# Optimization experiments

Measured on AMD Instinct MI355X. Metric: run time of the kernel, lower is better.

The kernel has to match this reference:

```python
import jax, jax.numpy as jnp
import numpy as np

N, K, S, E = 8192, 15, 128, 24
H, A, HID, DEPTH, MIX = 8, 32, 512, 3, 10
RBF_MAX, RBF_K = 20.0, 16


def _norm(v):
    return v / (jnp.linalg.norm(v, axis=-1, keepdims=True) + 1e-8)


def orientation_frames(pos):
    # pos: [N,3] CA coords -> per-residue local rotation frames [N,3,3]
    u = _norm(pos[1:] - pos[:-1])
    b = _norm(u[:-1] - u[1:])
    n = _norm(jnp.cross(u[:-1], u[1:]))
    o = jnp.cross(b, n)
    R = jnp.stack([b, n, o], axis=-1)              # [N-2,3,3]
    return jnp.concatenate([R[:1], R, R[-1:]], 0)  # edge-pad to [N,3,3]


def rot_to_quat(R):
    m00, m11, m22 = R[..., 0, 0], R[..., 1, 1], R[..., 2, 2]
    def comp(t, a, b):
        return 0.5 * jnp.sqrt(jnp.maximum(1e-8, t)) * jnp.sign(a - b)
    qw = 0.5 * jnp.sqrt(jnp.maximum(1e-8, 1. + m00 + m11 + m22))
    qx = comp(1. + m00 - m11 - m22, R[..., 2, 1], R[..., 1, 2])
    qy = comp(1. - m00 + m11 - m22, R[..., 0, 2], R[..., 2, 0])
    qz = comp(1. - m00 - m11 + m22, R[..., 1, 0], R[..., 0, 1])
    return jnp.stack([qw, qx, qy, qz], axis=-1)


def rbf_expand(d):
    mu = jnp.linspace(0., RBF_MAX, RBF_K)
    sigma = RBF_MAX / RBF_K
    return jnp.exp(-((d[..., None] - mu) / sigma) ** 2)


def layer_norm(x, g, b):
    m = x.mean(-1, keepdims=True)
    v = ((x - m) ** 2).mean(-1, keepdims=True)
    return (x - m) / jnp.sqrt(v + 1e-5) * g + b


def edge_features(pos, R, structure):
    # Target features are roll-by-1 of self (as in the torch forward's
    # distances.roll(1, dims=0)); sources are k-NN neighbours [N,K].
    inds = jnp.arange(N, dtype=pos.dtype)
    pos_t, R_t, ind_t = jnp.roll(pos, 1, 0), jnp.roll(R, 1, 0), jnp.roll(inds, 1, 0)
    pos_s, R_s, ind_s = pos[structure], R[structure], inds[structure]
    dvec = pos_s - pos_t[:, None]                    # [N,K,3]
    dist = jnp.linalg.norm(dvec, axis=-1)            # [N,K]
    direction = jnp.einsum('nji,nkj->nki', R_t, _norm(dvec))
    R_rel = jnp.einsum('nji,nkjl->nkil', R_t, R_s)   # R_t^T R_s
    quat = rot_to_quat(R_rel)                        # [N,K,4]
    rel_ind = (ind_s - ind_t[:, None])[..., None] / 100.0
    return jnp.concatenate([rbf_expand(dist), direction, quat, rel_ind], -1)  # [N,K,24]


def _forward(angles, tertiary, structure, W_in, b_in, W_pre, b_pre,
             ln1_g, ln1_b, Wq, bq, Wk, bk, Wv, bv, Wo, bo, ln2_g, ln2_b,
             W1, b1, W2, b2, W3, b3, Ws, bs, Wc, bc,
             W_conc, b_conc, W_wt, b_wt, W_fac, b_fac):
    prev = jnp.roll(angles, 1, 0).at[0].set(0.)
    afeat = jnp.concatenate([jnp.sin(prev), jnp.cos(prev)], -1)   # [N,6]
    feats = afeat @ W_in + b_in                                   # [N,S]
    pos = tertiary[:, 1]                                          # CA coords [N,3]
    R = orientation_frames(pos)
    edges = edge_features(pos, R, structure)                      # [N,K,E]
    x = feats @ W_pre + b_pre
    for d in range(DEPTH):
        nx = layer_norm(x, ln1_g[d], ln1_b[d])
        q = (nx @ Wq[d] + bq[d]).reshape(N, H, A)
        kv_in = jnp.concatenate([nx[structure], edges], -1)       # [N,K,S+E]
        k = (kv_in @ Wk[d] + bk[d]).reshape(N, K, H, A)
        v = (kv_in @ Wv[d] + bv[d]).reshape(N, K, H, A)
        logits = jnp.einsum('nha,nkha->nkh', q, k) / np.sqrt(A)
        attn = jax.nn.softmax(logits, axis=1)                     # over neighbours
        att = jnp.einsum('nkh,nkha->nha', attn, v).reshape(N, H * A) @ Wo[d] + bo[d]
        x = x + att
        h = layer_norm(x, ln2_g[d], ln2_b[d])
        h = jax.nn.relu(h @ W1[d] + b1[d])
        h = jax.nn.relu(h @ W2[d] + b2[d])
        x = x + (h @ W3[d] + b3[d])
    enc = x
    mean = jnp.arctan2(enc @ Ws + bs, enc @ Wc + bc).reshape(N, 3, MIX)
    factor = enc @ W_fac + b_fac
    mean = mean.at[:, 1].add((factor[:, 0] * angles[:, 0])[:, None])
    mean = mean.at[:, 2].add((factor[:, 1] * angles[:, 0] + factor[:, 2] * angles[:, 1])[:, None])
    conc = 0.1 + 1000. * jax.nn.sigmoid(enc @ W_conc + b_conc).reshape(N, 3, MIX)
    weights = jax.nn.softmax(enc @ W_wt + b_wt, axis=-1)
    return weights, mean, conc


def setup_inputs() -> dict:
    key = jax.random.key(0)
    ks = iter(jax.random.split(key, 64))
    def lin(i, o):
        return (jax.random.normal(next(ks), (i, o), jnp.float32) / np.sqrt(i),
                jnp.zeros((o,), jnp.float32))
    def stack_lin(i, o):
        w = jax.random.normal(next(ks), (DEPTH, i, o), jnp.float32) / np.sqrt(i)
        return w, jnp.zeros((DEPTH, o), jnp.float32)
    inp = {}
    inp['angles'] = jax.random.normal(next(ks), (N, 3), jnp.float32) * 1.5
    inp['tertiary'] = jax.random.normal(next(ks), (N, 3, 3), jnp.float32) * 3.0
    inp['structure'] = jax.random.randint(next(ks), (N, K), 0, N)
    inp['subgraph'] = jax.random.randint(next(ks), (N,), 0, 4)
    inp['W_in'], inp['b_in'] = lin(6, S)
    inp['W_pre'], inp['b_pre'] = lin(S, S)
    inp['ln1_g'] = jnp.ones((DEPTH, S)); inp['ln1_b'] = jnp.zeros((DEPTH, S))
    inp['ln2_g'] = jnp.ones((DEPTH, S)); inp['ln2_b'] = jnp.zeros((DEPTH, S))
    inp['Wq'], inp['bq'] = stack_lin(S, H * A)
    inp['Wk'], inp['bk'] = stack_lin(S + E, H * A)
    inp['Wv'], inp['bv'] = stack_lin(S + E, H * A)
    inp['Wo'], inp['bo'] = stack_lin(H * A, S)
    inp['W1'], inp['b1'] = stack_lin(S, HID)
    inp['W2'], inp['b2'] = stack_lin(HID, HID)
    inp['W3'], inp['b3'] = stack_lin(HID, S)
    inp['Ws'], inp['bs'] = lin(S, 3 * MIX)
    inp['Wc'], inp['bc'] = lin(S, 3 * MIX)
    inp['W_conc'], inp['b_conc'] = lin(S, 3 * MIX)
    inp['W_wt'], inp['b_wt'] = lin(S, MIX)
    inp['W_fac'], inp['b_fac'] = lin(S, 3)
    return inp


def reference(angles, tertiary, structure, subgraph, W_in, b_in, W_pre, b_pre,
              ln1_g, ln1_b, Wq, bq, Wk, bk, Wv, bv, Wo, bo, ln2_g, ln2_b,
              W1, b1, W2, b2, W3, b3, Ws, bs, Wc, bc,
              W_conc, b_conc, W_wt, b_wt, W_fac, b_fac):
    return _forward(angles, tertiary, structure, W_in, b_in, W_pre, b_pre,
                    ln1_g, ln1_b, Wq, bq, Wk, bk, Wv, bv, Wo, bo, ln2_g, ln2_b,
                    W1, b1, W2, b2, W3, b3, Ws, bs, Wc, bc,
                    W_conc, b_conc, W_wt, b_wt, W_fac, b_fac)
```

## Files before the change

### kernel.cpp

```cpp
#include <hip/hip_runtime.h>
#include <hip/hip_bf16.h>
#include <stdint.h>

#define NRES 8192
#define KNB  15
#define SDIM 128
#define EDIM 24
#define HIDD 512
#define NH   8
#define QDIM 256
#define MIXN 10

typedef _Float16 f16;
typedef _Float16 f16x8 __attribute__((ext_vector_type(8)));
typedef _Float16 f16x4 __attribute__((ext_vector_type(4)));
typedef _Float16 f16x2 __attribute__((ext_vector_type(2)));
typedef float f32x4 __attribute__((ext_vector_type(4)));

#if __has_builtin(__builtin_amdgcn_fdot2)
#define FDOT2(a,b,c) __builtin_amdgcn_fdot2((a),(b),(c),false)
#else
#define FDOT2(a,b,c) ((c) + (float)(a).x*(float)(b).x + (float)(a).y*(float)(b).y)
#endif

struct F3 { float x, y, z; };
__device__ __forceinline__ F3 f3sub(F3 a, F3 b) { return {a.x-b.x, a.y-b.y, a.z-b.z}; }
__device__ __forceinline__ F3 f3cross(F3 a, F3 b) {
  return {a.y*b.z - a.z*b.y, a.z*b.x - a.x*b.z, a.x*b.y - a.y*b.x};
}
__device__ __forceinline__ F3 f3norm(F3 a) {
  float l = sqrtf(a.x*a.x + a.y*a.y + a.z*a.z) + 1e-8f;
  float r = 1.f / l;
  return {a.x*r, a.y*r, a.z*r};
}
__device__ __forceinline__ F3 ldter(const float* t, int i) {
  return {t[i*9+3], t[i*9+4], t[i*9+5]};
}

__global__ void frames_kernel(const float* __restrict__ tert, float* __restrict__ R) {
  int m = blockIdx.x * blockDim.x + threadIdx.x;
  if (m >= NRES) return;
  int s = m - 1; if (s < 0) s = 0; if (s > NRES-3) s = NRES-3;
  F3 p0 = ldter(tert, s), p1 = ldter(tert, s+1), p2 = ldter(tert, s+2);
  F3 u0 = f3norm(f3sub(p1, p0));
  F3 u1 = f3norm(f3sub(p2, p1));
  F3 b  = f3norm(f3sub(u0, u1));
  F3 nn = f3norm(f3cross(u0, u1));
  F3 o  = f3cross(b, nn);
  float* r = R + m*9;
  r[0]=b.x; r[1]=nn.x; r[2]=o.x;
  r[3]=b.y; r[4]=nn.y; r[5]=o.y;
  r[6]=b.z; r[7]=nn.z; r[8]=o.z;
}

__device__ __forceinline__ float quat_comp(float t, float a, float b) {
  float s = (a > b) ? 1.f : ((a < b) ? -1.f : 0.f);
  return 0.5f * sqrtf(fmaxf(1e-8f, t)) * s;
}

__global__ void edges_kernel(const float* __restrict__ tert, const float* __restrict__ R,
                             const int* __restrict__ structure, f16* __restrict__ edges) {
  int id = blockIdx.x * blockDim.x + threadIdx.x;
  if (id >= NRES*KNB) return;
  int n = id / KNB;
  int tprev = (n - 1) & (NRES - 1);
  int sidx = structure[id];
  F3 pt = ldter(tert, tprev), ps = ldter(tert, sidx);
  F3 dv = f3sub(ps, pt);
  float dist = sqrtf(dv.x*dv.x + dv.y*dv.y + dv.z*dv.z);
  float rinv = 1.f / (dist + 1e-8f);
  F3 dh = {dv.x*rinv, dv.y*rinv, dv.z*rinv};
  float Rt[9], Rs[9];
#pragma unroll
  for (int i = 0; i < 9; i++) { Rt[i] = R[tprev*9+i]; Rs[i] = R[sidx*9+i]; }
  float dir[3];
#pragma unroll
  for (int i = 0; i < 3; i++) dir[i] = Rt[i]*dh.x + Rt[3+i]*dh.y + Rt[6+i]*dh.z;
  float Rr[9];
#pragma unroll
  for (int i = 0; i < 3; i++)
#pragma unroll
    for (int l = 0; l < 3; l++)
      Rr[i*3+l] = Rt[i]*Rs[l] + Rt[3+i]*Rs[3+l] + Rt[6+i]*Rs[6+l];
  float m00 = Rr[0], m11 = Rr[4], m22 = Rr[8];
  float qw = 0.5f * sqrtf(fmaxf(1e-8f, 1.f + m00 + m11 + m22));
  float qx = quat_comp(1.f + m00 - m11 - m22, Rr[7], Rr[5]);
  float qy = quat_comp(1.f - m00 + m11 - m22, Rr[2], Rr[6]);
  float qz = quat_comp(1.f - m00 - m11 + m22, Rr[3], Rr[1]);
  f16* e = edges + (size_t)id * EDIM;
#pragma unroll
  for (int j = 0; j < 16; j++) {
    float mu = (20.f / 15.f) * j;
    float zz = (dist - mu) * (1.f / 1.25f);
    e[j] = (f16)expf(-zz*zz);
  }
  e[16] = (f16)dir[0]; e[17] = (f16)dir[1]; e[18] = (f16)dir[2];
  e[19] = (f16)qw; e[20] = (f16)qx; e[21] = (f16)qy; e[22] = (f16)qz;
  e[23] = (f16)((float)(sidx - tprev) * 0.01f);
}

__global__ __launch_bounds__(128) void init_kernel(const float* __restrict__ angles,
    const float* __restrict__ W_in, const float* __restrict__ b_in,
    const float* __restrict__ W_pre, const float* __restrict__ b_pre, float* __restrict__ x) {
  int n = blockIdx.x, c = threadIdx.x;
  __shared__ float fs[128];
  float af[6];
  if (n == 0) { af[0]=af[1]=af[2]=0.f; af[3]=af[4]=af[5]=1.f; }
  else {
#pragma unroll
    for (int j = 0; j < 3; j++) {
      float p = angles[(n-1)*3 + j];
      af[j] = sinf(p); af[3+j] = cosf(p);
    }
  }
  float f = b_in[c];
#pragma unroll
  for (int j = 0; j < 6; j++) f += af[j] * W_in[j*SDIM + c];
  fs[c] = f;
  __syncthreads();
  float xv = b_pre[c];
  for (int j = 0; j < 128; j++) xv += fs[j] * W_pre[j*SDIM + c];
  x[(size_t)n*SDIM + c] = xv;
}

struct SwzJob { const float* src; int srcStride, srcLd, K, N; size_t dstOff; int dstLayerHalves, dstN, colOff; };
struct SwzJobs { SwzJob j[7]; };
__global__ void convswz_all(SwzJobs jobs, char* __restrict__ wsb) {
  SwzJob jb = jobs.j[blockIdx.y];
  int d = blockIdx.z;
  const float* s = jb.src + (size_t)d * jb.srcStride;
  f16* o = (f16*)(wsb + jb.dstOff) + (size_t)d * jb.dstLayerHalves;
  int tot = jb.K * jb.N;
  for (int i = blockIdx.x*blockDim.x + threadIdx.x; i < tot; i += gridDim.x*blockDim.x) {
    int k = i / jb.N, n = i - k*jb.N;
    o[((size_t)(k>>3)*jb.dstN + jb.colOff + n)*8 + (k&7)] = (f16)s[(size_t)k*jb.srcLd + n];
  }
}

__global__ __launch_bounds__(128) void wcomb_kernel(const float* __restrict__ Wq,
    const float* __restrict__ bq, const float* __restrict__ Wk, const float* __restrict__ bk,
    f16* __restrict__ qkvw, float* __restrict__ b1024) {
  int blk = blockIdx.x;
  int d = blk >> 8, col = blk & 255;
  int k = threadIdx.x;
  float acc = 0.f, bacc = 0.f;
  if (col < 200) {
    int h = col / 25, jj = col % 25;
    const float* WkB = Wk + (size_t)d*(SDIM+EDIM)*QDIM + (size_t)SDIM*QDIM;
    const float* wqrow = Wq + (size_t)d*SDIM*QDIM + (size_t)k*QDIM;
    int r0 = h*32;
    for (int rr = 0; rr < 32; rr++) {
      int r = r0 + rr;
      float wd = (jj < 24) ? WkB[(size_t)jj*QDIM + r] : bk[d*QDIM + r];
      acc += wqrow[r] * wd;
      if (k == 0) bacc += bq[d*QDIM + r] * wd;
    }
  }
  qkvw[(size_t)d*131072 + ((size_t)(k>>3)*1024 + 768 + col)*8 + (k&7)] = (f16)acc;
  if (k == 0) {
    b1024[d*1024 + col]       = bq[d*QDIM + col];
    b1024[d*1024 + 256 + col] = 0.f;
    b1024[d*1024 + 512 + col] = 0.f;
    b1024[d*1024 + 768 + col] = bacc;
  }
}

template<int MODE>
__global__ __launch_bounds__(256) void gemm_ln_mfma(const float* __restrict__ A,
    const float* __restrict__ lng, const float* __restrict__ lnb,
    const f16* __restrict__ Bsw, const float* __restrict__ bias,
    void* __restrict__ Cv, float* __restrict__ C2, int Nd) {
  int w = blockIdx.x * 4 + (threadIdx.x >> 6);
  int lane = threadIdx.x & 63;
  int wm = w & 255, wn = w >> 8;
  int m0 = wm * 32, n0 = wn * 64;
  int r16 = lane & 15, qd = lane >> 4;
  const float* r0p = A + (size_t)(m0 + r16)*SDIM + qd*8;
  const float* r1p = r0p + (size_t)16*SDIM;
  float4 a0[8], a1[8];
#pragma unroll
  for (int kc = 0; kc < 4; kc++) {
    a0[kc*2+0] = *(const float4*)(r0p + kc*32);
    a0[kc*2+1] = *(const float4*)(r0p + kc*32 + 4);
    a1[kc*2+0] = *(const float4*)(r1p + kc*32);
    a1[kc*2+1] = *(const float4*)(r1p + kc*32 + 4);
  }
  float s0 = 0.f, s1 = 0.f;
#pragma unroll
  for (int c = 0; c < 8; c++) {
    s0 += a0[c].x + a0[c].y + a0[c].z + a0[c].w;
    s1 += a1[c].x + a1[c].y + a1[c].z + a1[c].w;
  }
  s0 += __shfl_xor(s0, 16, 64); s0 += __shfl_xor(s0, 32, 64);
  s1 += __shfl_xor(s1, 16, 64); s1 += __shfl_xor(s1, 32, 64);
  float mean0 = s0 * (1.f/128.f), mean1 = s1 * (1.f/128.f);
  float v0 = 0.f, v1 = 0.f;
#pragma unroll
  for (int c = 0; c < 8; c++) {
    float d0x = a0[c].x-mean0, d0y = a0[c].y-mean0, d0z = a0[c].z-mean0, d0w = a0[c].w-mean0;
    v0 += d0x*d0x + d0y*d0y + d0z*d0z + d0w*d0w;
    float d1x = a1[c].x-mean1, d1y = a1[c].y-mean1, d1z = a1[c].z-mean1, d1w = a1[c].w-mean1;
    v1 += d1x*d1x + d1y*d1y + d1z*d1z + d1w*d1w;
  }
  v0 += __shfl_xor(v0, 16, 64); v0 += __shfl_xor(v0, 32, 64);
  v1 += __shfl_xor(v1, 16, 64); v1 += __shfl_xor(v1, 32, 64);
  float rs0 = rsqrtf(v0 * (1.f/128.f) + 1e-5f);
  float rs1 = rsqrtf(v1 * (1.f/128.f) + 1e-5f);
  f16x8 af0[4], af1[4];
#pragma unroll
  for (int kc = 0; kc < 4; kc++) {
    float4 g0 = *(const float4*)(lng + qd*8 + kc*32);
    float4 g1 = *(const float4*)(lng + qd*8 + kc*32 + 4);
    float4 bl0 = *(const float4*)(lnb + qd*8 + kc*32);
    float4 bl1 = *(const float4*)(lnb + qd*8 + kc*32 + 4);
    f16x8 f0, f1;
    f0[0] = (f16)((a0[kc*2].x  -mean0)*rs0*g0.x + bl0.x);
    f0[1] = (f16)((a0[kc*2].y  -mean0)*rs0*g0.y + bl0.y);
    f0[2] = (f16)((a0[kc*2].z  -mean0)*rs0*g0.z + bl0.z);
    f0[3] = (f16)((a0[kc*2].w  -mean0)*rs0*g0.w + bl0.w);
    f0[4] = (f16)((a0[kc*2+1].x-mean0)*rs0*g1.x + bl1.x);
    f0[5] = (f16)((a0[kc*2+1].y-mean0)*rs0*g1.y + bl1.y);
    f0[6] = (f16)((a0[kc*2+1].z-mean0)*rs0*g1.z + bl1.z);
    f0[7] = (f16)((a0[kc*2+1].w-mean0)*rs0*g1.w + bl1.w);
    f1[0] = (f16)((a1[kc*2].x  -mean1)*rs1*g0.x + bl0.x);
    f1[1] = (f16)((a1[kc*2].y  -mean1)*rs1*g0.y + bl0.y);
    f1[2] = (f16)((a1[kc*2].z  -mean1)*rs1*g0.z + bl0.z);
    f1[3] = (f16)((a1[kc*2].w  -mean1)*rs1*g0.w + bl0.w);
    f1[4] = (f16)((a1[kc*2+1].x-mean1)*rs1*g1.x + bl1.x);
    f1[5] = (f16)((a1[kc*2+1].y-mean1)*rs1*g1.y + bl1.y);
    f1[6] = (f16)((a1[kc*2+1].z-mean1)*rs1*g1.z + bl1.z);
    f1[7] = (f16)((a1[kc*2+1].w-mean1)*rs1*g1.w + bl1.w);
    af0[kc] = f0; af1[kc] = f1;
  }
  f32x4 acc[2][4] = {};
#pragma unroll
  for (int kc = 0; kc < 4; kc++) {
    const f16* bBase = Bsw + ((size_t)(kc*4 + qd)*Nd + n0 + r16)*8;
    f16x8 bf[4];
#pragma unroll
    for (int nt = 0; nt < 4; nt++) bf[nt] = *(const f16x8*)(bBase + nt*16*8);
#pragma unroll
    for (int nt = 0; nt < 4; nt++) {
      acc[0][nt] = __builtin_amdgcn_mfma_f32_16x16x32_f16(af0[kc], bf[nt], acc[0][nt], 0, 0, 0);
      acc[1][nt] = __builtin_amdgcn_mfma_f32_16x16x32_f16(af1[kc], bf[nt], acc[1][nt], 0, 0, 0);
    }
  }
#pragma unroll
  for (int mt = 0; mt < 2; mt++) {
#pragma unroll
    for (int nt = 0; nt < 4; nt++) {
      int col = n0 + nt*16 + r16;
      float bj = bias[col];
#pragma unroll
      for (int r = 0; r < 4; r++) {
        int row = m0 + mt*16 + qd*4 + r;
        float v = acc[mt][nt][r] + bj;
        if (MODE == 1) {
          ((f16*)Cv)[(size_t)row*Nd + col] = (f16)fmaxf(v, 0.f);
        } else {
          int third = col >> 8, cl = col & 255;
          if (third < 3)
            ((f16*)Cv)[(size_t)third*NRES*QDIM + (size_t)row*QDIM + cl] = (f16)v;
          else
            C2[(size_t)row*256 + cl] = v;
        }
      }
    }
  }
}

__global__ __launch_bounds__(256) void ffn2_kernel(const f16* __restrict__ att,
    const f16* __restrict__ wosw, const float* __restrict__ bo,
    const float* __restrict__ xin,
    const float* __restrict__ lng, const float* __restrict__ lnb,
    const f16* __restrict__ w1sw, const float* __restrict__ b1,
    const f16* __restrict__ w2sw, const float* __restrict__ b2,
    const f16* __restrict__ w3sw, const float* __restrict__ b3,
    float* __restrict__ xout) {
  __shared__ float xs[16][132];
  __shared__ f16 h1s[16][520];
  __shared__ f16 h2s[16][520];
  int wv = threadIdx.x >> 6;
  int lane = threadIdx.x & 63;
  int m0 = blockIdx.x * 16;
  int r16 = lane & 15, qd = lane >> 4;

  {
    f32x4 acc[2] = {};
    const f16* aBase = att + (size_t)(m0 + r16)*QDIM + qd*8;
    for (int kc = 0; kc < QDIM; kc += 32) {
      f16x8 af = *(const f16x8*)(aBase + kc);
      const f16* bBase = wosw + ((size_t)((kc>>3) + qd)*SDIM + wv*32 + r16)*8;
#pragma unroll
      for (int nt = 0; nt < 2; nt++) {
        f16x8 bf = *(const f16x8*)(bBase + nt*16*8);
        acc[nt] = __builtin_amdgcn_mfma_f32_16x16x32_f16(af, bf, acc[nt], 0, 0, 0);
      }
    }
#pragma unroll
    for (int nt = 0; nt < 2; nt++) {
      int col = wv*32 + nt*16 + r16;
      float bj = bo[col];
#pragma unroll
      for (int r = 0; r < 4; r++) {
        int rl = qd*4 + r;
        xs[rl][col] = xin[(size_t)(m0 + rl)*SDIM + col] + acc[nt][r] + bj;
      }
    }
  }
  __syncthreads();

  float4 a0[8];
#pragma unroll
  for (int kc = 0; kc < 4; kc++) {
    a0[kc*2+0] = *(const float4*)&xs[r16][qd*8 + kc*32];
    a0[kc*2+1] = *(const float4*)&xs[r16][qd*8 + kc*32 + 4];
  }
  float s0 = 0.f;
#pragma unroll
  for (int c = 0; c < 8; c++) s0 += a0[c].x + a0[c].y + a0[c].z + a0[c].w;
  s0 += __shfl_xor(s0, 16, 64); s0 += __shfl_xor(s0, 32, 64);
  float mean0 = s0 * (1.f/128.f);
  float v0 = 0.f;
#pragma unroll
  for (int c = 0; c < 8; c++) {
    float dx = a0[c].x-mean0, dy = a0[c].y-mean0, dz = a0[c].z-mean0, dw = a0[c].w-mean0;
    v0 += dx*dx + dy*dy + dz*dz + dw*dw;
  }
  v0 += __shfl_xor(v0, 16, 64); v0 += __shfl_xor(v0, 32, 64);
  float rs0 = rsqrtf(v0 * (1.f/128.f) + 1e-5f);
  f16x8 af[4];
#pragma unroll
  for (int kc = 0; kc < 4; kc++) {
    float4 g0 = *(const float4*)(lng + qd*8 + kc*32);
    float4 g1 = *(const float4*)(lng + qd*8 + kc*32 + 4);
    float4 bl0 = *(const float4*)(lnb + qd*8 + kc*32);
    float4 bl1 = *(const float4*)(lnb + qd*8 + kc*32 + 4);
    f16x8 f0;
    f0[0] = (f16)((a0[kc*2].x  -mean0)*rs0*g0.x + bl0.x);
    f0[1] = (f16)((a0[kc*2].y  -mean0)*rs0*g0.y + bl0.y);
    f0[2] = (f16)((a0[kc*2].z  -mean0)*rs0*g0.z + bl0.z);
    f0[3] = (f16)((a0[kc*2].w  -mean0)*rs0*g0.w + bl0.w);
    f0[4] = (f16)((a0[kc*2+1].x-mean0)*rs0*g1.x + bl1.x);
    f0[5] = (f16)((a0[kc*2+1].y-mean0)*rs0*g1.y + bl1.y);
    f0[6] = (f16)((a0[kc*2+1].z-mean0)*rs0*g1.z + bl1.z);
    f0[7] = (f16)((a0[kc*2+1].w-mean0)*rs0*g1.w + bl1.w);
    af[kc] = f0;
  }
  {
    f32x4 acc[8] = {};
#pragma unroll
    for (int kc = 0; kc < 4; kc++) {
      const f16* bBase = w1sw + ((size_t)(kc*4 + qd)*HIDD + wv*128 + r16)*8;
#pragma unroll
      for (int nt = 0; nt < 8; nt++) {
        f16x8 bf = *(const f16x8*)(bBase + nt*16*8);
        acc[nt] = __builtin_amdgcn_mfma_f32_16x16x32_f16(af[kc], bf, acc[nt], 0, 0, 0);
      }
    }
#pragma unroll
    for (int nt = 0; nt < 8; nt++) {
      int col = wv*128 + nt*16 + r16;
      float bj = b1[col];
#pragma unroll
      for (int r = 0; r < 4; r++)
        h1s[qd*4 + r][col] = (f16)fmaxf(acc[nt][r] + bj, 0.f);
    }
  }
  __syncthreads();
  {
    f32x4 acc[8] = {};
    for (int kc = 0; kc < 16; kc++) {
      f16x8 a = *(const f16x8*)&h1s[r16][qd*8 + kc*32];
      const f16* bBase = w2sw + ((size_t)(kc*4 + qd)*HIDD + wv*128 + r16)*8;
#pragma unroll
      for (int nt = 0; nt < 8; nt++) {
        f16x8 bf = *(const f16x8*)(bBase + nt*16*8);
        acc[nt] = __builtin_amdgcn_mfma_f32_16x16x32_f16(a, bf, acc[nt], 0, 0, 0);
      }
    }
#pragma unroll
    for (int nt = 0; nt < 8; nt++) {
      int col = wv*128 + nt*16 + r16;
      float bj = b2[col];
#pragma unroll
      for (int r = 0; r < 4; r++)
        h2s[qd*4 + r][col] = (f16)fmaxf(acc[nt][r] + bj, 0.f);
    }
  }
  __syncthreads();
  {
    f32x4 acc[2] = {};
    for (int kc = 0; kc < 16; kc++) {
      f16x8 a = *(const f16x8*)&h2s[r16][qd*8 + kc*32];
      const f16* bBase = w3sw + ((size_t)(kc*4 + qd)*SDIM + wv*32 + r16)*8;
#pragma unroll
      for (int nt = 0; nt < 2; nt++) {
        f16x8 bf = *(const f16x8*)(bBase + nt*16*8);
        acc[nt] = __builtin_amdgcn_mfma_f32_16x16x32_f16(a, bf, acc[nt], 0, 0, 0);
      }
    }
#pragma unroll
    for (int nt = 0; nt < 2; nt++) {
      int col = wv*32 + nt*16 + r16;
      float bj = b3[col];
#pragma unroll
      for (int r = 0; r < 4; r++) {
        int rl = qd*4 + r;
        xout[(size_t)(m0 + rl)*SDIM + col] = xs[rl][col] + acc[nt][r] + bj;
      }
    }
  }
}

__global__ __launch_bounds__(256) void attn_kernel(const f16* __restrict__ q,
    const f16* __restrict__ pk, const f16* __restrict__ pv,
    const f16* __restrict__ edges, const int* __restrict__ structure,
    const float* __restrict__ qW, const float* __restrict__ WvB,
    const float* __restrict__ bv, f16* __restrict__ att) {
  int t = threadIdx.x;
  int n = blockIdx.x*4 + (t >> 6);
  int lane = t & 63;
  int h = lane >> 3, i = lane & 7, base = h << 3;

  int s[KNB];
#pragma unroll
  for (int kk = 0; kk < KNB; kk++) s[kk] = structure[n*KNB + kk];
  const f16x4* pk4 = (const f16x4*)pk;
  const f16x4* pv4 = (const f16x4*)pv;
  f16x4 pks[KNB], pvs[KNB];
#pragma unroll
  for (int kk = 0; kk < KNB; kk++) pks[kk] = pk4[(size_t)s[kk]*64 + lane];
#pragma unroll
  for (int kk = 0; kk < KNB; kk++) pvs[kk] = pv4[(size_t)s[kk]*64 + lane];
  f16x4 q4 = ((const f16x4*)q)[(size_t)n*64 + lane];

  const float* qwr = qW + (size_t)n*256 + h*25;
  float qbias = qwr[24];
  float elA = qbias, elB = qbias;
  {
    const f16x2* eA = (const f16x2*)(edges + (size_t)n*KNB*EDIM + i*EDIM);
#pragma unroll
    for (int j2 = 0; j2 < 12; j2++) {
      f16x2 e2 = eA[j2];
      elA += qwr[2*j2]*(float)e2.x + qwr[2*j2+1]*(float)e2.y;
    }
  }
  if (i < 7) {
    const f16x2* eB = (const f16x2*)(edges + (size_t)n*KNB*EDIM + (i+8)*EDIM);
#pragma unroll
    for (int j2 = 0; j2 < 12; j2++) {
      f16x2 e2 = eB[j2];
      elB += qwr[2*j2]*(float)e2.x + qwr[2*j2+1]*(float)e2.y;
    }
  }

  float dot[KNB];
  f16x2 qlo; qlo.x = q4.x; qlo.y = q4.y;
  f16x2 qhi; qhi.x = q4.z; qhi.y = q4.w;
#pragma unroll
  for (int kk = 0; kk < KNB; kk++) {
    f16x2 plo; plo.x = pks[kk].x; plo.y = pks[kk].y;
    f16x2 phi; phi.x = pks[kk].z; phi.y = pks[kk].w;
    float p = FDOT2(qlo, plo, 0.f);
    p = FDOT2(qhi, phi, p);
    p += __shfl_xor(p, 4, 64);
    p += __shfl_xor(p, 2, 64);
    p += __shfl_xor(p, 1, 64);
    dot[kk] = p;
  }

  float logit[KNB];
#pragma unroll
  for (int kk = 0; kk < 8; kk++) {
    float el = __shfl(elA, base + kk, 64);
    logit[kk] = (dot[kk] + el) * 0.17677669529663687f;
  }
#pragma unroll
  for (int kk = 8; kk < KNB; kk++) {
    float el = __shfl(elB, base + (kk - 8), 64);
    logit[kk] = (dot[kk] + el) * 0.17677669529663687f;
  }

  float mx = -1e30f;
#pragma unroll
  for (int kk = 0; kk < KNB; kk++) mx = fmaxf(mx, logit[kk]);
  float attw[KNB]; float sum = 0.f;
#pragma unroll
  for (int kk = 0; kk < KNB; kk++) { attw[kk] = expf(logit[kk] - mx); sum += attw[kk]; }
  float inv = 1.f / sum;
#pragma unroll
  for (int kk = 0; kk < KNB; kk++) attw[kk] *= inv;

  float4 o = ((const float4*)bv)[lane];
#pragma unroll
  for (int kk = 0; kk < KNB; kk++) {
    float a = attw[kk];
    o.x += a * (float)pvs[kk].x;
    o.y += a * (float)pvs[kk].y;
    o.z += a * (float)pvs[kk].z;
    o.w += a * (float)pvs[kk].w;
  }

  const f16* ebase = edges + (size_t)n*KNB*EDIM;
  float ew0 = 0.f, ew1 = 0.f, ew2 = 0.f;
#pragma unroll
  for (int kk = 0; kk < KNB; kk++) {
    float a = attw[kk];
    ew0 += a * (float)ebase[kk*EDIM + 3*i + 0];
    ew1 += a * (float)ebase[kk*EDIM + 3*i + 1];
    ew2 += a * (float)ebase[kk*EDIM + 3*i + 2];
  }

#pragma unroll
  for (int src = 0; src < 8; src++) {
    float w0 = __shfl(ew0, base + src, 64);
    float w1 = __shfl(ew1, base + src, 64);
    float w2 = __shfl(ew2, base + src, 64);
    float4 wv0 = ((const float4*)(WvB + (size_t)(3*src + 0)*QDIM))[lane];
    float4 wv1 = ((const float4*)(WvB + (size_t)(3*src + 1)*QDIM))[lane];
    float4 wv2 = ((const float4*)(WvB + (size_t)(3*src + 2)*QDIM))[lane];
    o.x += w0*wv0.x + w1*wv1.x + w2*wv2.x;
    o.y += w0*wv0.y + w1*wv1.y + w2*wv2.y;
    o.z += w0*wv0.z + w1*wv1.z + w2*wv2.z;
    o.w += w0*wv0.w + w1*wv1.w + w2*wv2.w;
  }

  f16x4 ov; ov.x = (f16)o.x; ov.y = (f16)o.y; ov.z = (f16)o.z; ov.w = (f16)o.w;
  ((f16x4*)att)[(size_t)n*64 + lane] = ov;
}

__global__ __launch_bounds__(128) void head_kernel(const float* __restrict__ enc,
    const float* Ws, const float* bs, const float* Wc, const float* bc,
    const float* Wconc, const float* bconc, const float* Wwt, const float* bwt,
    const float* Wfac, const float* bfac, const float* __restrict__ angles, float* __restrict__ out) {
  int n = blockIdx.x, t = threadIdx.x;
  __shared__ float es[128];
  __shared__ float outs[103];
  es[t] = enc[(size_t)n*SDIM + t];
  __syncthreads();
  const float* W = nullptr; const float* bb = nullptr; int col = 0, nc = 0;
  if (t < 30)       { W = Ws;    bb = bs;    col = t;       nc = 30; }
  else if (t < 60)  { W = Wc;    bb = bc;    col = t - 30;  nc = 30; }
  else if (t < 90)  { W = Wconc; bb = bconc; col = t - 60;  nc = 30; }
  else if (t < 100) { W = Wwt;   bb = bwt;   col = t - 90;  nc = 10; }
  else if (t < 103) { W = Wfac;  bb = bfac;  col = t - 100; nc = 3;  }
  if (W) {
    float acc = bb[col];
    for (int j = 0; j < 128; j++) acc += es[j] * W[j*nc + col];
    outs[t] = acc;
  }
  __syncthreads();
  if (t < MIXN) {
    float mx = -1e30f;
    for (int m = 0; m < MIXN; m++) mx = fmaxf(mx, outs[90 + m]);
    float sum = 0.f;
    for (int m = 0; m < MIXN; m++) sum += expf(outs[90 + m] - mx);
    out[(size_t)n*MIXN + t] = expf(outs[90 + t] - mx) / sum;
  }
  if (t < 30) {
    int j = t / 10;
    float v = atan2f(outs[t], outs[30 + t]);
    float a0 = angles[n*3 + 0], a1 = angles[n*3 + 1];
    if (j == 1) v += outs[100] * a0;
    if (j == 2) v += outs[101] * a0 + outs[102] * a1;
    out[(size_t)NRES*MIXN + (size_t)n*30 + t] = v;
    float z = outs[60 + t];
    float sg = 1.f / (1.f + expf(-z));
    out[(size_t)NRES*MIXN + (size_t)NRES*30 + (size_t)n*30 + t] = 0.1f + 1000.f * sg;
  }
}

extern "C" void kernel_launch(void* const* d_in, const int* in_sizes, int n_in,
                              void* d_out, int out_size, void* d_ws, size_t ws_size,
                              hipStream_t stream) {
  const float* angles   = (const float*)d_in[0];
  const float* tertiary = (const float*)d_in[1];
  const int*   structure = (const int*)d_in[2];
  const float* W_in  = (const float*)d_in[4];  const float* b_in  = (const float*)d_in[5];
  const float* W_pre = (const float*)d_in[6];  const float* b_pre = (const float*)d_in[7];
  const float* ln1_g = (const float*)d_in[8];  const float* ln1_b = (const float*)d_in[9];
  const float* ln2_g = (const float*)d_in[10]; const float* ln2_b = (const float*)d_in[11];
  const float* Wq = (const float*)d_in[12]; const float* bq = (const float*)d_in[13];
  const float* Wk = (const float*)d_in[14]; const float* bk = (const float*)d_in[15];
  const float* Wv = (const float*)d_in[16]; const float* bv = (const float*)d_in[17];
  const float* Wo = (const float*)d_in[18]; const float* bo = (const float*)d_in[19];
  const float* W1 = (const float*)d_in[20]; const float* b1 = (const float*)d_in[21];
  const float* W2 = (const float*)d_in[22]; const float* b2 = (const float*)d_in[23];
  const float* W3 = (const float*)d_in[24]; const float* b3 = (const float*)d_in[25];
  const float* Ws = (const float*)d_in[26]; const float* bs = (const float*)d_in[27];
  const float* Wc = (const float*)d_in[28]; const float* bc = (const float*)d_in[29];
  const float* Wconc = (const float*)d_in[30]; const float* bconc = (const float*)d_in[31];
  const float* Wwt = (const float*)d_in[32]; const float* bwt = (const float*)d_in[33];
  const float* Wfac = (const float*)d_in[34]; const float* bfac = (const float*)d_in[35];

  char* wsb = (char*)d_ws;
  float* Rm    = (float*)(wsb + 0);
  f16*   edg_h = (f16*)  (wsb + 294912);
  float* x     = (float*)(wsb + 6193152);
  f16*   att_h = (f16*)  (wsb + 10387456);
  f16*   qh    = (f16*)  (wsb + 14581760);
  f16*   pkh   = (f16*)  (wsb + 18776064);
  f16*   pvh   = (f16*)  (wsb + 22970368);
  size_t qkvwOff = 27164672;
  size_t w1wOff  = 27951104;
  size_t w2wOff  = 28344320;
  size_t w3wOff  = 29917184;
  size_t wowOff  = 30310400;
  f16*   qkvw  = (f16*)(wsb + qkvwOff);
  f16*   w1w   = (f16*)(wsb + w1wOff);
  f16*   w2w   = (f16*)(wsb + w2wOff);
  f16*   w3w   = (f16*)(wsb + w3wOff);
  f16*   wow   = (f16*)(wsb + wowOff);
  float* b1024 = (float*)(wsb + 30507008);
  float* qWb   = (float*)(wsb + 30519296);

  frames_kernel<<<dim3((NRES+255)/256), dim3(256), 0, stream>>>(tertiary, Rm);
  edges_kernel<<<dim3((NRES*KNB+255)/256), dim3(256), 0, stream>>>(tertiary, Rm, structure, edg_h);
  init_kernel<<<dim3(NRES), dim3(128), 0, stream>>>(angles, W_in, b_in, W_pre, b_pre, x);

  SwzJobs jobs;
  jobs.j[0] = { Wq, SDIM*QDIM,        QDIM, 128, 256, qkvwOff, 131072, 1024, 0   };
  jobs.j[1] = { Wk, (SDIM+EDIM)*QDIM, QDIM, 128, 256, qkvwOff, 131072, 1024, 256 };
  jobs.j[2] = { Wv, (SDIM+EDIM)*QDIM, QDIM, 128, 256, qkvwOff, 131072, 1024, 512 };
  jobs.j[3] = { W1, SDIM*HIDD, HIDD, 128, 512, w1wOff, 65536,  512, 0 };
  jobs.j[4] = { W2, HIDD*HIDD, HIDD, 512, 512, w2wOff, 262144, 512, 0 };
  jobs.j[5] = { W3, HIDD*SDIM, SDIM, 512, 128, w3wOff, 65536,  128, 0 };
  jobs.j[6] = { Wo, QDIM*SDIM, SDIM, 256, 128, wowOff, 32768,  128, 0 };
  convswz_all<<<dim3(64, 7, 3), dim3(256), 0, stream>>>(jobs, wsb);
  wcomb_kernel<<<768, 128, 0, stream>>>(Wq, bq, Wk, bk, qkvw, b1024);

  for (int d = 0; d < 3; ++d) {
    const float* WvD = Wv + (size_t)d*(SDIM+EDIM)*QDIM;
    gemm_ln_mfma<3><<<1024, 256, 0, stream>>>(x, ln1_g + d*SDIM, ln1_b + d*SDIM,
        qkvw + (size_t)d*131072, b1024 + d*1024, qh, qWb, 1024);
    attn_kernel<<<dim3(NRES/4), dim3(256), 0, stream>>>(qh, pkh, pvh, edg_h, structure,
        qWb, WvD + (size_t)SDIM*QDIM, bv + d*QDIM, att_h);
    ffn2_kernel<<<dim3(NRES/16), dim3(256), 0, stream>>>(att_h,
        wow + (size_t)d*32768, bo + d*SDIM, x,
        ln2_g + d*SDIM, ln2_b + d*SDIM,
        w1w + (size_t)d*65536, b1 + d*HIDD,
        w2w + (size_t)d*262144, b2 + d*HIDD,
        w3w + (size_t)d*65536, b3 + d*SDIM, x);
  }

  head_kernel<<<dim3(NRES), dim3(128), 0, stream>>>(x, Ws, bs, Wc, bc, Wconc, bconc,
      Wwt, bwt, Wfac, bfac, angles, (float*)d_out);
}
```

Measured before the change: 416.4 us.

## Split ffn2 across eight waves and fold weight-combine into swizzle launch

The FFN kernel now runs 512 threads (8 waves) per 16-row block, with each wave computing half as many output columns in every GEMM stage. This shortens each wave's serial MFMA chain and adds latency hiding, at the cost of more waves per block and more shared-memory sync participants. Separately, the Wq·Wk combine kernel is merged into the weight-swizzle kernel as an extra grid slice, removing one launch.

```diff
diff --git a/kernel.cpp b/kernel.cpp
--- a/kernel.cpp
+++ b/kernel.cpp
@@ -125,43 +125,46 @@
 
 struct SwzJob { const float* src; int srcStride, srcLd, K, N; size_t dstOff; int dstLayerHalves, dstN, colOff; };
 struct SwzJobs { SwzJob j[7]; };
-__global__ void convswz_all(SwzJobs jobs, char* __restrict__ wsb) {
+__global__ void convswz_all(SwzJobs jobs, char* __restrict__ wsb,
+    const float* __restrict__ Wq, const float* __restrict__ bq,
+    const float* __restrict__ Wk, const float* __restrict__ bk,
+    size_t qkvwOff, size_t b1024Off) {
+  int d = blockIdx.z;
+  if (blockIdx.y == 7) {
+    f16* qkvw = (f16*)(wsb + qkvwOff);
+    float* b1024 = (float*)(wsb + b1024Off);
+    for (int i = blockIdx.x*blockDim.x + threadIdx.x; i < 256*128; i += gridDim.x*blockDim.x) {
+      int col = i >> 7, k = i & 127;
+      float acc = 0.f, bacc = 0.f;
+      if (col < 200) {
+        int h = col / 25, jj = col % 25;
+        const float* WkB = Wk + (size_t)d*(SDIM+EDIM)*QDIM + (size_t)SDIM*QDIM;
+        const float* wqrow = Wq + (size_t)d*SDIM*QDIM + (size_t)k*QDIM;
+        int r0 = h*32;
+        for (int rr = 0; rr < 32; rr++) {
+          int r = r0 + rr;
+          float wd = (jj < 24) ? WkB[(size_t)jj*QDIM + r] : bk[d*QDIM + r];
+          acc += wqrow[r] * wd;
+          if (k == 0) bacc += bq[d*QDIM + r] * wd;
+        }
+      }
+      qkvw[(size_t)d*131072 + ((size_t)(k>>3)*1024 + 768 + col)*8 + (k&7)] = (f16)acc;
+      if (k == 0) {
+        b1024[d*1024 + col]       = bq[d*QDIM + col];
+        b1024[d*1024 + 256 + col] = 0.f;
+        b1024[d*1024 + 512 + col] = 0.f;
+        b1024[d*1024 + 768 + col] = bacc;
+      }
+    }
+    return;
+  }
   SwzJob jb = jobs.j[blockIdx.y];
-  int d = blockIdx.z;
   const float* s = jb.src + (size_t)d * jb.srcStride;
   f16* o = (f16*)(wsb + jb.dstOff) + (size_t)d * jb.dstLayerHalves;
   int tot = jb.K * jb.N;
   for (int i = blockIdx.x*blockDim.x + threadIdx.x; i < tot; i += gridDim.x*blockDim.x) {
     int k = i / jb.N, n = i - k*jb.N;
     o[((size_t)(k>>3)*jb.dstN + jb.colOff + n)*8 + (k&7)] = (f16)s[(size_t)k*jb.srcLd + n];
-  }
-}
-
-__global__ __launch_bounds__(128) void wcomb_kernel(const float* __restrict__ Wq,
-    const float* __restrict__ bq, const float* __restrict__ Wk, const float* __restrict__ bk,
-    f16* __restrict__ qkvw, float* __restrict__ b1024) {
-  int blk = blockIdx.x;
-  int d = blk >> 8, col = blk & 255;
-  int k = threadIdx.x;
-  float acc = 0.f, bacc = 0.f;
-  if (col < 200) {
-    int h = col / 25, jj = col % 25;
-    const float* WkB = Wk + (size_t)d*(SDIM+EDIM)*QDIM + (size_t)SDIM*QDIM;
-    const float* wqrow = Wq + (size_t)d*SDIM*QDIM + (size_t)k*QDIM;
-    int r0 = h*32;
-    for (int rr = 0; rr < 32; rr++) {
-      int r = r0 + rr;
-      float wd = (jj < 24) ? WkB[(size_t)jj*QDIM + r] : bk[d*QDIM + r];
-      acc += wqrow[r] * wd;
-      if (k == 0) bacc += bq[d*QDIM + r] * wd;
-    }
-  }
-  qkvw[(size_t)d*131072 + ((size_t)(k>>3)*1024 + 768 + col)*8 + (k&7)] = (f16)acc;
-  if (k == 0) {
-    b1024[d*1024 + col]       = bq[d*QDIM + col];
-    b1024[d*1024 + 256 + col] = 0.f;
-    b1024[d*1024 + 512 + col] = 0.f;
-    b1024[d*1024 + 768 + col] = bacc;
   }
 }
 
@@ -269,7 +272,7 @@
   }
 }
 
-__global__ __launch_bounds__(256) void ffn2_kernel(const f16* __restrict__ att,
+__global__ __launch_bounds__(512) void ffn2_kernel(const f16* __restrict__ att,
     const f16* __restrict__ wosw, const float* __restrict__ bo,
     const float* __restrict__ xin,
     const float* __restrict__ lng, const float* __restrict__ lnb,
@@ -286,26 +289,19 @@
   int r16 = lane & 15, qd = lane >> 4;
 
   {
-    f32x4 acc[2] = {};
+    f32x4 acc = {};
     const f16* aBase = att + (size_t)(m0 + r16)*QDIM + qd*8;
     for (int kc = 0; kc < QDIM; kc += 32) {
       f16x8 af = *(const f16x8*)(aBase + kc);
-      const f16* bBase = wosw + ((size_t)((kc>>3) + qd)*SDIM + wv*32 + r16)*8;
-#pragma unroll
-      for (int nt = 0; nt < 2; nt++) {
-        f16x8 bf = *(const f16x8*)(bBase + nt*16*8);
-        acc[nt] = __builtin_amdgcn_mfma_f32_16x16x32_f16(af, bf, acc[nt], 0, 0, 0);
-      }
-    }
-#pragma unroll
-    for (int nt = 0; nt < 2; nt++) {
-      int col = wv*32 + nt*16 + r16;
-      float bj = bo[col];
-#pragma unroll
-      for (int r = 0; r < 4; r++) {
-        int rl = qd*4 + r;
-        xs[rl][col] = xin[(size_t)(m0 + rl)*SDIM + col] + acc[nt][r] + bj;
-      }
+      f16x8 bf = *(const f16x8*)(wosw + ((size_t)((kc>>3) + qd)*SDIM + wv*16 + r16)*8);
+      acc = __builtin_amdgcn_mfma_f32_16x16x32_f16(af, bf, acc, 0, 0, 0);
+    }
+    int col = wv*16 + r16;
+    float bj = bo[col];
+#pragma unroll
+    for (int r = 0; r < 4; r++) {
+      int rl = qd*4 + r;
+      xs[rl][col] = xin[(size_t)(m0 + rl)*SDIM + col] + acc[r] + bj;
     }
   }
   __syncthreads();
@@ -348,19 +344,19 @@
     af[kc] = f0;
   }
   {
-    f32x4 acc[8] = {};
+    f32x4 acc[4] = {};
 #pragma unroll
     for (int kc = 0; kc < 4; kc++) {
-      const f16* bBase = w1sw + ((size_t)(kc*4 + qd)*HIDD + wv*128 + r16)*8;
-#pragma unroll
-      for (int nt = 0; nt < 8; nt++) {
+      const f16* bBase = w1sw + ((size_t)(kc*4 + qd)*HIDD + wv*64 + r16)*8;
+#pragma unroll
+      for (int nt = 0; nt < 4; nt++) {
         f16x8 bf = *(const f16x8*)(bBase + nt*16*8);
         acc[nt] = __builtin_amdgcn_mfma_f32_16x16x32_f16(af[kc], bf, acc[nt], 0, 0, 0);
       }
     }
 #pragma unroll
-    for (int nt = 0; nt < 8; nt++) {
-      int col = wv*128 + nt*16 + r16;
+    for (int nt = 0; nt < 4; nt++) {
+      int col = wv*64 + nt*16 + r16;
       float bj = b1[col];
 #pragma unroll
       for (int r = 0; r < 4; r++)
@@ -369,19 +365,19 @@
   }
   __syncthreads();
   {
-    f32x4 acc[8] = {};
+    f32x4 acc[4] = {};
     for (int kc = 0; kc < 16; kc++) {
       f16x8 a = *(const f16x8*)&h1s[r16][qd*8 + kc*32];
-      const f16* bBase = w2sw + ((size_t)(kc*4 + qd)*HIDD + wv*128 + r16)*8;
-#pragma unroll
-      for (int nt = 0; nt < 8; nt++) {
+      const f16* bBase = w2sw + ((size_t)(kc*4 + qd)*HIDD + wv*64 + r16)*8;
+#pragma unroll
+      for (int nt = 0; nt < 4; nt++) {
         f16x8 bf = *(const f16x8*)(bBase + nt*16*8);
         acc[nt] = __builtin_amdgcn_mfma_f32_16x16x32_f16(a, bf, acc[nt], 0, 0, 0);
       }
     }
 #pragma unroll
-    for (int nt = 0; nt < 8; nt++) {
-      int col = wv*128 + nt*16 + r16;
+    for (int nt = 0; nt < 4; nt++) {
+      int col = wv*64 + nt*16 + r16;
       float bj = b2[col];
 #pragma unroll
       for (int r = 0; r < 4; r++)
@@ -390,25 +386,18 @@
   }
   __syncthreads();
   {
-    f32x4 acc[2] = {};
+    f32x4 acc = {};
     for (int kc = 0; kc < 16; kc++) {
       f16x8 a = *(const f16x8*)&h2s[r16][qd*8 + kc*32];
-      const f16* bBase = w3sw + ((size_t)(kc*4 + qd)*SDIM + wv*32 + r16)*8;
-#pragma unroll
-      for (int nt = 0; nt < 2; nt++) {
-        f16x8 bf = *(const f16x8*)(bBase + nt*16*8);
-        acc[nt] = __builtin_amdgcn_mfma_f32_16x16x32_f16(a, bf, acc[nt], 0, 0, 0);
-      }
-    }
-#pragma unroll
-    for (int nt = 0; nt < 2; nt++) {
-      int col = wv*32 + nt*16 + r16;
-      float bj = b3[col];
-#pragma unroll
-      for (int r = 0; r < 4; r++) {
-        int rl = qd*4 + r;
-        xout[(size_t)(m0 + rl)*SDIM + col] = xs[rl][col] + acc[nt][r] + bj;
-      }
+      f16x8 bf = *(const f16x8*)(w3sw + ((size_t)(kc*4 + qd)*SDIM + wv*16 + r16)*8);
+      acc = __builtin_amdgcn_mfma_f32_16x16x32_f16(a, bf, acc, 0, 0, 0);
+    }
+    int col = wv*16 + r16;
+    float bj = b3[col];
+#pragma unroll
+    for (int r = 0; r < 4; r++) {
+      int rl = qd*4 + r;
+      xout[(size_t)(m0 + rl)*SDIM + col] = xs[rl][col] + acc[r] + bj;
     }
   }
 }
@@ -612,8 +601,9 @@
   f16*   w2w   = (f16*)(wsb + w2wOff);
   f16*   w3w   = (f16*)(wsb + w3wOff);
   f16*   wow   = (f16*)(wsb + wowOff);
-  float* b1024 = (float*)(wsb + 30507008);
+  size_t b1024Off = 30507008;
   float* qWb   = (float*)(wsb + 30519296);
+  float* b1024 = (float*)(wsb + b1024Off);
 
   frames_kernel<<<dim3((NRES+255)/256), dim3(256), 0, stream>>>(tertiary, Rm);
   edges_kernel<<<dim3((NRES*KNB+255)/256), dim3(256), 0, stream>>>(tertiary, Rm, structure, edg_h);
@@ -627,8 +617,8 @@
   jobs.j[4] = { W2, HIDD*HIDD, HIDD, 512, 512, w2wOff, 262144, 512, 0 };
   jobs.j[5] = { W3, HIDD*SDIM, SDIM, 512, 128, w3wOff, 65536,  128, 0 };
   jobs.j[6] = { Wo, QDIM*SDIM, SDIM, 256, 128, wowOff, 32768,  128, 0 };
-  convswz_all<<<dim3(64, 7, 3), dim3(256), 0, stream>>>(jobs, wsb);
-  wcomb_kernel<<<768, 128, 0, stream>>>(Wq, bq, Wk, bk, qkvw, b1024);
+  convswz_all<<<dim3(64, 8, 3), dim3(256), 0, stream>>>(jobs, wsb, Wq, bq, Wk, bk,
+      qkvwOff, b1024Off);
 
   for (int d = 0; d < 3; ++d) {
     const float* WvD = Wv + (size_t)d*(SDIM+EDIM)*QDIM;
@@ -636,7 +626,7 @@
         qkvw + (size_t)d*131072, b1024 + d*1024, qh, qWb, 1024);
     attn_kernel<<<dim3(NRES/4), dim3(256), 0, stream>>>(qh, pkh, pvh, edg_h, structure,
         qWb, WvD + (size_t)SDIM*QDIM, bv + d*QDIM, att_h);
-    ffn2_kernel<<<dim3(NRES/16), dim3(256), 0, stream>>>(att_h,
+    ffn2_kernel<<<dim3(NRES/16), dim3(512), 0, stream>>>(att_h,
         wow + (size_t)d*32768, bo + d*SDIM, x,
         ln2_g + d*SDIM, ln2_b + d*SDIM,
         w1w + (size_t)d*65536, b1 + d*HIDD,
```

Result: slower. 431.0 us (+3.5%).
